# Kernel tuning notes

Hardware: AMD Instinct MI355X
Metric: run time of the kernel (lower is better)

The kernel has to match this reference:

```python
import jax, jax.numpy as jnp
import numpy as np

N_NODES = 100000
N_EDGES = 800000
F_DIM = 64
N_GRAPHS = 64


def _gcn_layer(h, W, b, src, dst, dis):
    # h: [N, F]; symmetric-normalized GCN conv with self-loops (PyG GCNConv semantics)
    hw = h @ W                                   # dense projection [N, F]
    norm = dis[src] * dis[dst]                   # [E]
    agg = jax.ops.segment_sum(hw[src] * norm[:, None], dst, num_segments=N_NODES)
    agg = agg + (dis * dis)[:, None] * hw        # self-loop contribution
    return agg + b


def setup_inputs() -> dict:
    key = jax.random.key(0)
    ks = jax.random.split(key, 10)
    x = jax.random.normal(ks[0], (N_NODES, F_DIM), dtype=jnp.float32)
    edge_index = jax.random.randint(ks[1], (2, N_EDGES), 0, N_NODES, dtype=jnp.int64 if jax.config.jax_enable_x64 else jnp.int32)
    batch = jnp.sort(jax.random.randint(ks[2], (N_NODES,), 0, N_GRAPHS, dtype=jnp.int32))
    scale = 1.0 / np.sqrt(F_DIM)
    W1 = jax.random.normal(ks[3], (F_DIM, F_DIM), dtype=jnp.float32) * scale
    b1 = jnp.zeros((F_DIM,), dtype=jnp.float32)
    W2 = jax.random.normal(ks[4], (F_DIM, F_DIM), dtype=jnp.float32) * scale
    b2 = jnp.zeros((F_DIM,), dtype=jnp.float32)
    W3 = jax.random.normal(ks[5], (F_DIM, F_DIM), dtype=jnp.float32) * scale
    b3 = jnp.zeros((F_DIM,), dtype=jnp.float32)
    return {"x": x, "edge_index": edge_index, "batch": batch,
            "W1": W1, "b1": b1, "W2": W2, "b2": b2, "W3": W3, "b3": b3}


def reference(x, edge_index, batch, W1, b1, W2, b2, W3, b3):
    src, dst = edge_index[0], edge_index[1]
    # degree with self-loops: deg[i] = 1 + in-degree(i)
    deg = jax.ops.segment_sum(jnp.ones((N_EDGES,), dtype=x.dtype), dst, num_segments=N_NODES) + 1.0
    dis = jax.lax.rsqrt(deg)                     # deg >= 1 always
    h = jax.nn.relu(_gcn_layer(x, W1, b1, src, dst, dis))
    h = jax.nn.relu(_gcn_layer(h, W2, b2, src, dst, dis))
    h = _gcn_layer(h, W3, b3, src, dst, dis)
    # global max pool over graphs in the batch
    out = jax.ops.segment_max(h, batch, num_segments=N_GRAPHS)
    return out
```

## Files before the change

### kernel.cpp

```cpp
#include <hip/hip_runtime.h>
#include <math.h>

#define N_NODES  100000
#define N_EDGES  800000
#define F        64
#define N_GRAPHS 64
#define NQUADS   25000
#define ROWB     128

typedef _Float16 half8 __attribute__((ext_vector_type(8)));
typedef float    f32x4 __attribute__((ext_vector_type(4)));

#define OFF_BUFA 0u
#define OFF_BUFB 12800256u
#define OFF_DIS  25600512u
#define OFF_DEG  26000512u
#define OFF_QB   26400512u
#define OFF_BSUM 26500544u
#define OFF_COL  26501120u
#define OFF_WT   40501120u

__device__ inline ushort f2bf(float f) {
    uint u = __float_as_uint(f);
    u = (u + 0x7FFFu + ((u >> 16) & 1u)) >> 16;
    return (ushort)u;
}
__device__ inline float bf2f(ushort s) {
    return __uint_as_float(((uint)s) << 16);
}

__global__ void k_zero(int* __restrict__ p, int n) {
    int i = blockIdx.x * blockDim.x + threadIdx.x;
    if (i < n) p[i] = 0;
}

__global__ void k_degree(const int* __restrict__ dst, int* __restrict__ degcnt,
                         int* __restrict__ rank) {
    int e = blockIdx.x * blockDim.x + threadIdx.x;
    if (e < N_EDGES) rank[e] = atomicAdd(&degcnt[dst[e]], 1);
}

__global__ void k_quad(const int* __restrict__ degcnt, int* __restrict__ qbase,
                       int* __restrict__ bsum, float* __restrict__ dis) {
    __shared__ int s[1024];
    int q = blockIdx.x * 1024 + threadIdx.x;
    int tot = 0;
    if (q < NQUADS) {
        const int4 d4 = *(const int4*)(degcnt + q * 4);
        float4 dv;
        dv.x = rsqrtf((float)d4.x + 1.0f);
        dv.y = rsqrtf((float)d4.y + 1.0f);
        dv.z = rsqrtf((float)d4.z + 1.0f);
        dv.w = rsqrtf((float)d4.w + 1.0f);
        *(float4*)(dis + q * 4) = dv;
        int m = max(max(d4.x, d4.y), max(d4.z, d4.w));
        int P = (m + 3) & ~3;
        tot = 4 * P;
    }
    s[threadIdx.x] = tot;
    __syncthreads();
    for (int off = 1; off < 1024; off <<= 1) {
        int t = (threadIdx.x >= off) ? s[threadIdx.x - off] : 0;
        __syncthreads();
        s[threadIdx.x] += t;
        __syncthreads();
    }
    if (q < NQUADS) qbase[q + 1] = s[threadIdx.x];
    if (threadIdx.x == 1023) bsum[blockIdx.x] = s[1023];
}

__global__ void k_scan2(int* __restrict__ bsum, int nb) {
    __shared__ int s[128];
    int t = threadIdx.x;
    int v = (t < nb) ? bsum[t] : 0;
    s[t] = v;
    __syncthreads();
    for (int off = 1; off < 128; off <<= 1) {
        int u = (t >= off) ? s[t - off] : 0;
        __syncthreads();
        s[t] += u;
        __syncthreads();
    }
    if (t < nb) bsum[t] = s[t] - v;
}

__global__ void k_scan3(int* __restrict__ qbase, const int* __restrict__ bsum) {
    int q = blockIdx.x * 1024 + threadIdx.x;
    if (q < NQUADS) qbase[q + 1] += bsum[blockIdx.x];
    if (q == 0) qbase[0] = 0;
}

__global__ void k_colinit(const int* __restrict__ qbase, int* __restrict__ col) {
    int total = qbase[NQUADS];
    int stride = gridDim.x * blockDim.x;
    for (int i = blockIdx.x * blockDim.x + threadIdx.x; i < total; i += stride)
        col[i] = N_NODES * ROWB;
}

__global__ void k_fill(const int* __restrict__ src, const int* __restrict__ dst,
                       const int* __restrict__ qbase, const int* __restrict__ rank,
                       int* __restrict__ col) {
    int e = blockIdx.x * blockDim.x + threadIdx.x;
    if (e < N_EDGES) {
        int d = dst[e];
        col[qbase[d >> 2] + rank[e] * 4 + (d & 3)] = src[e] * ROWB;
    }
}

__global__ void k_prepx(const float* __restrict__ x, const float* __restrict__ dis,
                        ushort* __restrict__ xs) {
    int t = blockIdx.x * blockDim.x + threadIdx.x;
    if (t < N_NODES * 8) {
        int n = t >> 3;
        float d = dis[n];
        const float4* px = (const float4*)(x + (size_t)t * 8);
        float4 a = px[0], b = px[1];
        ushort o[8] = { f2bf(d*a.x), f2bf(d*a.y), f2bf(d*a.z), f2bf(d*a.w),
                        f2bf(d*b.x), f2bf(d*b.y), f2bf(d*b.z), f2bf(d*b.w) };
        *(uint4*)(xs + (size_t)t * 8) = *(const uint4*)o;
    }
}

__global__ void k_prepw(const float* __restrict__ W1, const float* __restrict__ W2,
                        const float* __restrict__ W3, _Float16* __restrict__ Wt,
                        ushort* __restrict__ bufA, ushort* __restrict__ bufB,
                        float* __restrict__ out) {
    int t = blockIdx.x * blockDim.x + threadIdx.x;
    if (t < 3 * 4096) {
        int wsel = t >> 12, i = t & 4095;
        int k = i >> 6, f = i & 63;
        const float* Ws = (wsel == 0) ? W1 : (wsel == 1) ? W2 : W3;
        Wt[wsel * 4096 + f * 64 + k] = (_Float16)Ws[k * 64 + f];
    } else if (t < 3 * 4096 + 64) {
        int f = t - 3 * 4096;
        bufA[(size_t)N_NODES * F + f] = 0;
        bufB[(size_t)N_NODES * F + f] = 0;
    } else if (t < 3 * 4096 + 64 + N_GRAPHS * F) {
        out[t - (3 * 4096 + 64)] = -INFINITY;
    }
}

template<bool RELU, bool SCALE>
__global__ __launch_bounds__(256) void k_layer(const ushort* __restrict__ hs,
                                               const int* __restrict__ qbase,
                                               const int* __restrict__ col,
                                               const float* __restrict__ dis,
                                               const _Float16* __restrict__ Wt,
                                               const float* __restrict__ bias,
                                               ushort* __restrict__ hout) {
    __shared__ _Float16 g[64 * 64];
    int lane = threadIdx.x & 63;
    int w    = __builtin_amdgcn_readfirstlane(threadIdx.x >> 6);
    int chunk = blockIdx.x * 64;
    int wr16 = w * 16;
    int nbase = chunk + wr16;
    const char* hsb = (const char*)hs;
    int l2 = lane << 1;

    for (int p = 0; p < 4; ++p) {
        int na = nbase + 4 * p;
        int quad = na >> 2;
        int rowb = wr16 + 4 * p;
        bool vq = quad < NQUADS;
        int qb0 = 0, iters = 0;
        if (vq) {
            qb0   = __builtin_amdgcn_readfirstlane(qbase[quad]);
            int qb1 = __builtin_amdgcn_readfirstlane(qbase[quad + 1]);
            iters = (qb1 - qb0) >> 4;
        }
        float a0 = vq ? bf2f(hs[(size_t)(na    ) * F + lane]) : 0.f;
        float a1 = vq ? bf2f(hs[(size_t)(na + 1) * F + lane]) : 0.f;
        float a2 = vq ? bf2f(hs[(size_t)(na + 2) * F + lane]) : 0.f;
        float a3 = vq ? bf2f(hs[(size_t)(na + 3) * F + lane]) : 0.f;
        const int* cp0 = col + qb0;
        for (int i = 0; i < iters; ++i) {
            const int* cp = cp0 + (i << 4);
            float v0  = bf2f(*(const ushort*)(hsb + (uint)cp[0]  + l2));
            float v1  = bf2f(*(const ushort*)(hsb + (uint)cp[1]  + l2));
            float v2  = bf2f(*(const ushort*)(hsb + (uint)cp[2]  + l2));
            float v3  = bf2f(*(const ushort*)(hsb + (uint)cp[3]  + l2));
            float v4  = bf2f(*(const ushort*)(hsb + (uint)cp[4]  + l2));
            float v5  = bf2f(*(const ushort*)(hsb + (uint)cp[5]  + l2));
            float v6  = bf2f(*(const ushort*)(hsb + (uint)cp[6]  + l2));
            float v7  = bf2f(*(const ushort*)(hsb + (uint)cp[7]  + l2));
            float v8  = bf2f(*(const ushort*)(hsb + (uint)cp[8]  + l2));
            float v9  = bf2f(*(const ushort*)(hsb + (uint)cp[9]  + l2));
            float v10 = bf2f(*(const ushort*)(hsb + (uint)cp[10] + l2));
            float v11 = bf2f(*(const ushort*)(hsb + (uint)cp[11] + l2));
            float v12 = bf2f(*(const ushort*)(hsb + (uint)cp[12] + l2));
            float v13 = bf2f(*(const ushort*)(hsb + (uint)cp[13] + l2));
            float v14 = bf2f(*(const ushort*)(hsb + (uint)cp[14] + l2));
            float v15 = bf2f(*(const ushort*)(hsb + (uint)cp[15] + l2));
            a0 += v0 + v4 + v8  + v12;
            a1 += v1 + v5 + v9  + v13;
            a2 += v2 + v6 + v10 + v14;
            a3 += v3 + v7 + v11 + v15;
        }
        float d0 = vq ? dis[na]     : 0.f;
        float d1 = vq ? dis[na + 1] : 0.f;
        float d2 = vq ? dis[na + 2] : 0.f;
        float d3 = vq ? dis[na + 3] : 0.f;
        g[(rowb    ) * 64 + lane] = (_Float16)(d0 * a0);
        g[(rowb + 1) * 64 + lane] = (_Float16)(d1 * a1);
        g[(rowb + 2) * 64 + lane] = (_Float16)(d2 * a2);
        g[(rowb + 3) * 64 + lane] = (_Float16)(d3 * a3);
    }

    int l15 = lane & 15, lh = lane >> 4;
    half8 bfrag[2][4];
#pragma unroll
    for (int ks = 0; ks < 2; ++ks)
#pragma unroll
        for (int nt = 0; nt < 4; ++nt)
            bfrag[ks][nt] = *(const half8*)(Wt + (nt * 16 + l15) * 64 + ks * 32 + lh * 8);

    f32x4 acc4[4] = {};
#pragma unroll
    for (int ks = 0; ks < 2; ++ks) {
        half8 a = *(const half8*)(&g[(wr16 + l15) * 64 + ks * 32 + lh * 8]);
#pragma unroll
        for (int nt = 0; nt < 4; ++nt)
            acc4[nt] = __builtin_amdgcn_mfma_f32_16x16x32_f16(a, bfrag[ks][nt], acc4[nt], 0, 0, 0);
    }

    float bvals[4];
#pragma unroll
    for (int nt = 0; nt < 4; ++nt) bvals[nt] = bias[nt * 16 + l15];
#pragma unroll
    for (int rr = 0; rr < 4; ++rr) {
        int row = wr16 + lh * 4 + rr;
        int ng = chunk + row;
        if (ng < N_NODES) {
            float ds2 = 1.f;
            if (SCALE) ds2 = dis[ng];
#pragma unroll
            for (int nt = 0; nt < 4; ++nt) {
                float vv = acc4[nt][rr] + bvals[nt];
                if (RELU) vv = fmaxf(vv, 0.f);
                if (SCALE) vv *= ds2;
                hout[(size_t)ng * F + nt * 16 + l15] = f2bf(vv);
            }
        }
    }
}

__device__ inline void atomicMaxFloat(float* addr, float v) {
    if (v >= 0.f) atomicMax((int*)addr, __float_as_int(v));
    else          atomicMin((unsigned int*)addr, __float_as_uint(v));
}

__global__ __launch_bounds__(256) void k_pool(const ushort* __restrict__ h,
                                              const int* __restrict__ batch,
                                              float* __restrict__ out) {
    int lane = threadIdx.x & 63;
    int wid  = __builtin_amdgcn_readfirstlane((blockIdx.x * blockDim.x + threadIdx.x) >> 6);
    int nwaves = (gridDim.x * blockDim.x) >> 6;
    int per = (N_NODES + nwaves - 1) / nwaves;
    int n0 = wid * per, n1 = min(N_NODES, n0 + per);
    if (n0 >= n1) return;
    float acc = -INFINITY;
    int cur = batch[n0];
    for (int n = n0; n < n1; ++n) {
        int g = batch[n];
        if (g != cur) {
            atomicMaxFloat(&out[cur * F + lane], acc);
            acc = -INFINITY; cur = g;
        }
        acc = fmaxf(acc, bf2f(h[(size_t)n * F + lane]));
    }
    atomicMaxFloat(&out[cur * F + lane], acc);
}

extern "C" void kernel_launch(void* const* d_in, const int* in_sizes, int n_in,
                              void* d_out, int out_size, void* d_ws, size_t ws_size,
                              hipStream_t stream) {
    const float* x     = (const float*)d_in[0];
    const int*   ei    = (const int*)d_in[1];
    const int*   batch = (const int*)d_in[2];
    const float* W1 = (const float*)d_in[3];
    const float* b1 = (const float*)d_in[4];
    const float* W2 = (const float*)d_in[5];
    const float* b2 = (const float*)d_in[6];
    const float* W3 = (const float*)d_in[7];
    const float* b3 = (const float*)d_in[8];
    const int* src = ei;
    const int* dst = ei + N_EDGES;

    char* ws = (char*)d_ws;
    ushort*   bufA   = (ushort*)(ws + OFF_BUFA);
    int*      rank   = (int*)(ws + OFF_BUFA);
    ushort*   bufB   = (ushort*)(ws + OFF_BUFB);
    float*    dis    = (float*)(ws + OFF_DIS);
    int*      degcnt = (int*)(ws + OFF_DEG);
    int*      qbase  = (int*)(ws + OFF_QB);
    int*      bsum   = (int*)(ws + OFF_BSUM);
    int*      col    = (int*)(ws + OFF_COL);
    _Float16* wt     = (_Float16*)(ws + OFF_WT);
    float*    out    = (float*)d_out;

    k_zero<<<(N_NODES + 255) / 256, 256, 0, stream>>>(degcnt, N_NODES);
    k_degree<<<(N_EDGES + 255) / 256, 256, 0, stream>>>(dst, degcnt, rank);
    k_quad<<<25, 1024, 0, stream>>>(degcnt, qbase, bsum, dis);
    k_scan2<<<1, 128, 0, stream>>>(bsum, 25);
    k_scan3<<<25, 1024, 0, stream>>>(qbase, bsum);
    k_colinit<<<1024, 256, 0, stream>>>(qbase, col);
    k_fill<<<(N_EDGES + 255) / 256, 256, 0, stream>>>(src, dst, qbase, rank, col);

    k_prepx<<<(N_NODES * 8 + 255) / 256, 256, 0, stream>>>(x, dis, bufA);
    k_prepw<<<65, 256, 0, stream>>>(W1, W2, W3, wt, bufA, bufB, out);

    const int LBLOCKS = (N_NODES + 63) / 64;
    k_layer<true,  true ><<<LBLOCKS, 256, 0, stream>>>(bufA, qbase, col, dis, wt,        b1, bufB);
    k_layer<true,  true ><<<LBLOCKS, 256, 0, stream>>>(bufB, qbase, col, dis, wt + 4096, b2, bufA);
    k_layer<false, false><<<LBLOCKS, 256, 0, stream>>>(bufA, qbase, col, dis, wt + 8192, b3, bufB);

    k_pool<<<512, 256, 0, stream>>>(bufB, batch, out);
}
```

Before: 181.1 us.

## Fuse setup kernels and fold global max pool into final layer

Merges degree zeroing, column-sentinel init, weight transpose and output init into one kernel. Folds the second-level scan into the scan-apply kernel, which now also runs the input prescale. Fuses the graph max-pool into the last GCN layer using shared-memory atomics per block, so the final activations are never written or reread. This cuts launch count and one full pass over node features. In exchange, col is now initialised to a fixed capacity rather than the exact size, rank moves to its own buffer, and the pool relies on sorted batch ids with at most four graphs per block before falling back to global atomics.

```diff
diff --git a/kernel.cpp b/kernel.cpp
--- a/kernel.cpp
+++ b/kernel.cpp
@@ -7,6 +7,8 @@
 #define N_GRAPHS 64
 #define NQUADS   25000
 #define ROWB     128
+#define COLCAP   3500000
+#define SENT     (N_NODES * ROWB)
 
 typedef _Float16 half8 __attribute__((ext_vector_type(8)));
 typedef float    f32x4 __attribute__((ext_vector_type(4)));
@@ -19,6 +21,7 @@
 #define OFF_BSUM 26500544u
 #define OFF_COL  26501120u
 #define OFF_WT   40501120u
+#define OFF_RANK 40525696u
 
 __device__ inline ushort f2bf(float f) {
     uint u = __float_as_uint(f);
@@ -29,9 +32,32 @@
     return __uint_as_float(((uint)s) << 16);
 }
 
-__global__ void k_zero(int* __restrict__ p, int n) {
-    int i = blockIdx.x * blockDim.x + threadIdx.x;
-    if (i < n) p[i] = 0;
+__device__ inline void atomicMaxFloat(float* addr, float v) {
+    if (v >= 0.f) atomicMax((int*)addr, __float_as_int(v));
+    else          atomicMin((unsigned int*)addr, __float_as_uint(v));
+}
+
+__global__ void k_init(const float* __restrict__ W1, const float* __restrict__ W2,
+                       const float* __restrict__ W3, _Float16* __restrict__ Wt,
+                       ushort* __restrict__ bufA, ushort* __restrict__ bufB,
+                       float* __restrict__ out, int* __restrict__ degcnt,
+                       int* __restrict__ col) {
+    int tid = blockIdx.x * blockDim.x + threadIdx.x;
+    int stride = gridDim.x * blockDim.x;
+    for (int i = tid; i < COLCAP; i += stride) col[i] = SENT;
+    for (int i = tid; i < N_NODES; i += stride) degcnt[i] = 0;
+    if (tid < 3 * 4096) {
+        int wsel = tid >> 12, i = tid & 4095;
+        int k = i >> 6, f = i & 63;
+        const float* Ws = (wsel == 0) ? W1 : (wsel == 1) ? W2 : W3;
+        Wt[wsel * 4096 + f * 64 + k] = (_Float16)Ws[k * 64 + f];
+    } else if (tid < 3 * 4096 + 64) {
+        int f = tid - 3 * 4096;
+        bufA[(size_t)N_NODES * F + f] = 0;
+        bufB[(size_t)N_NODES * F + f] = 0;
+    } else if (tid < 3 * 4096 + 64 + N_GRAPHS * F) {
+        out[tid - (3 * 4096 + 64)] = -INFINITY;
+    }
 }
 
 __global__ void k_degree(const int* __restrict__ dst, int* __restrict__ degcnt,
@@ -69,32 +95,33 @@
     if (threadIdx.x == 1023) bsum[blockIdx.x] = s[1023];
 }
 
-__global__ void k_scan2(int* __restrict__ bsum, int nb) {
-    __shared__ int s[128];
-    int t = threadIdx.x;
-    int v = (t < nb) ? bsum[t] : 0;
-    s[t] = v;
-    __syncthreads();
-    for (int off = 1; off < 128; off <<= 1) {
-        int u = (t >= off) ? s[t - off] : 0;
+__global__ void k_scan3px(int* __restrict__ qbase, const int* __restrict__ bsum,
+                          const float* __restrict__ x, const float* __restrict__ dis,
+                          ushort* __restrict__ xs) {
+    if (blockIdx.x < 25) {
+        __shared__ int soff;
+        if (threadIdx.x == 0) {
+            int acc = 0;
+            for (int j = 0; j < (int)blockIdx.x; ++j) acc += bsum[j];
+            soff = acc;
+        }
         __syncthreads();
-        s[t] += u;
-        __syncthreads();
-    }
-    if (t < nb) bsum[t] = s[t] - v;
-}
-
-__global__ void k_scan3(int* __restrict__ qbase, const int* __restrict__ bsum) {
-    int q = blockIdx.x * 1024 + threadIdx.x;
-    if (q < NQUADS) qbase[q + 1] += bsum[blockIdx.x];
-    if (q == 0) qbase[0] = 0;
-}
-
-__global__ void k_colinit(const int* __restrict__ qbase, int* __restrict__ col) {
-    int total = qbase[NQUADS];
-    int stride = gridDim.x * blockDim.x;
-    for (int i = blockIdx.x * blockDim.x + threadIdx.x; i < total; i += stride)
-        col[i] = N_NODES * ROWB;
+        int off = soff;
+        int q = blockIdx.x * 1024 + threadIdx.x;
+        if (q < NQUADS) qbase[q + 1] += off;
+        if (q == 0) qbase[0] = 0;
+    } else {
+        int t = (blockIdx.x - 25) * 1024 + threadIdx.x;
+        if (t < N_NODES * 8) {
+            int n = t >> 3;
+            float d = dis[n];
+            const float4* px = (const float4*)(x + (size_t)t * 8);
+            float4 a = px[0], b = px[1];
+            ushort o[8] = { f2bf(d*a.x), f2bf(d*a.y), f2bf(d*a.z), f2bf(d*a.w),
+                            f2bf(d*b.x), f2bf(d*b.y), f2bf(d*b.z), f2bf(d*b.w) };
+            *(uint4*)(xs + (size_t)t * 8) = *(const uint4*)o;
+        }
+    }
 }
 
 __global__ void k_fill(const int* __restrict__ src, const int* __restrict__ dst,
@@ -107,48 +134,18 @@
     }
 }
 
-__global__ void k_prepx(const float* __restrict__ x, const float* __restrict__ dis,
-                        ushort* __restrict__ xs) {
-    int t = blockIdx.x * blockDim.x + threadIdx.x;
-    if (t < N_NODES * 8) {
-        int n = t >> 3;
-        float d = dis[n];
-        const float4* px = (const float4*)(x + (size_t)t * 8);
-        float4 a = px[0], b = px[1];
-        ushort o[8] = { f2bf(d*a.x), f2bf(d*a.y), f2bf(d*a.z), f2bf(d*a.w),
-                        f2bf(d*b.x), f2bf(d*b.y), f2bf(d*b.z), f2bf(d*b.w) };
-        *(uint4*)(xs + (size_t)t * 8) = *(const uint4*)o;
-    }
-}
-
-__global__ void k_prepw(const float* __restrict__ W1, const float* __restrict__ W2,
-                        const float* __restrict__ W3, _Float16* __restrict__ Wt,
-                        ushort* __restrict__ bufA, ushort* __restrict__ bufB,
-                        float* __restrict__ out) {
-    int t = blockIdx.x * blockDim.x + threadIdx.x;
-    if (t < 3 * 4096) {
-        int wsel = t >> 12, i = t & 4095;
-        int k = i >> 6, f = i & 63;
-        const float* Ws = (wsel == 0) ? W1 : (wsel == 1) ? W2 : W3;
-        Wt[wsel * 4096 + f * 64 + k] = (_Float16)Ws[k * 64 + f];
-    } else if (t < 3 * 4096 + 64) {
-        int f = t - 3 * 4096;
-        bufA[(size_t)N_NODES * F + f] = 0;
-        bufB[(size_t)N_NODES * F + f] = 0;
-    } else if (t < 3 * 4096 + 64 + N_GRAPHS * F) {
-        out[t - (3 * 4096 + 64)] = -INFINITY;
-    }
-}
-
-template<bool RELU, bool SCALE>
+template<bool RELU, bool SCALE, bool POOL>
 __global__ __launch_bounds__(256) void k_layer(const ushort* __restrict__ hs,
                                                const int* __restrict__ qbase,
                                                const int* __restrict__ col,
                                                const float* __restrict__ dis,
                                                const _Float16* __restrict__ Wt,
                                                const float* __restrict__ bias,
-                                               ushort* __restrict__ hout) {
+                                               ushort* __restrict__ hout,
+                                               const int* __restrict__ batch,
+                                               float* __restrict__ out) {
     __shared__ _Float16 g[64 * 64];
+    __shared__ float pl[4 * 64];
     int lane = threadIdx.x & 63;
     int w    = __builtin_amdgcn_readfirstlane(threadIdx.x >> 6);
     int chunk = blockIdx.x * 64;
@@ -156,6 +153,8 @@
     int nbase = chunk + wr16;
     const char* hsb = (const char*)hs;
     int l2 = lane << 1;
+
+    if (POOL) pl[threadIdx.x] = -INFINITY;
 
     for (int p = 0; p < 4; ++p) {
         int na = nbase + 4 * p;
@@ -226,49 +225,47 @@
     float bvals[4];
 #pragma unroll
     for (int nt = 0; nt < 4; ++nt) bvals[nt] = bias[nt * 16 + l15];
+
+    if (POOL) __syncthreads();
+    int gmin = 0;
+    if (POOL) gmin = __builtin_amdgcn_readfirstlane(batch[chunk]);
+
 #pragma unroll
     for (int rr = 0; rr < 4; ++rr) {
         int row = wr16 + lh * 4 + rr;
         int ng = chunk + row;
         if (ng < N_NODES) {
-            float ds2 = 1.f;
-            if (SCALE) ds2 = dis[ng];
-#pragma unroll
-            for (int nt = 0; nt < 4; ++nt) {
-                float vv = acc4[nt][rr] + bvals[nt];
-                if (RELU) vv = fmaxf(vv, 0.f);
-                if (SCALE) vv *= ds2;
-                hout[(size_t)ng * F + nt * 16 + l15] = f2bf(vv);
+            if (POOL) {
+                int gb = batch[ng];
+                int rel = gb - gmin;
+#pragma unroll
+                for (int nt = 0; nt < 4; ++nt) {
+                    float vv = acc4[nt][rr] + bvals[nt];
+                    if (RELU) vv = fmaxf(vv, 0.f);
+                    if (rel < 4) atomicMaxFloat(&pl[rel * 64 + nt * 16 + l15], vv);
+                    else         atomicMaxFloat(&out[gb * F + nt * 16 + l15], vv);
+                }
+            } else {
+                float ds2 = 1.f;
+                if (SCALE) ds2 = dis[ng];
+#pragma unroll
+                for (int nt = 0; nt < 4; ++nt) {
+                    float vv = acc4[nt][rr] + bvals[nt];
+                    if (RELU) vv = fmaxf(vv, 0.f);
+                    if (SCALE) vv *= ds2;
+                    hout[(size_t)ng * F + nt * 16 + l15] = f2bf(vv);
+                }
             }
         }
     }
-}
-
-__device__ inline void atomicMaxFloat(float* addr, float v) {
-    if (v >= 0.f) atomicMax((int*)addr, __float_as_int(v));
-    else          atomicMin((unsigned int*)addr, __float_as_uint(v));
-}
-
-__global__ __launch_bounds__(256) void k_pool(const ushort* __restrict__ h,
-                                              const int* __restrict__ batch,
-                                              float* __restrict__ out) {
-    int lane = threadIdx.x & 63;
-    int wid  = __builtin_amdgcn_readfirstlane((blockIdx.x * blockDim.x + threadIdx.x) >> 6);
-    int nwaves = (gridDim.x * blockDim.x) >> 6;
-    int per = (N_NODES + nwaves - 1) / nwaves;
-    int n0 = wid * per, n1 = min(N_NODES, n0 + per);
-    if (n0 >= n1) return;
-    float acc = -INFINITY;
-    int cur = batch[n0];
-    for (int n = n0; n < n1; ++n) {
-        int g = batch[n];
-        if (g != cur) {
-            atomicMaxFloat(&out[cur * F + lane], acc);
-            acc = -INFINITY; cur = g;
-        }
-        acc = fmaxf(acc, bf2f(h[(size_t)n * F + lane]));
-    }
-    atomicMaxFloat(&out[cur * F + lane], acc);
+    if (POOL) {
+        __syncthreads();
+        float v = pl[threadIdx.x];
+        int r = threadIdx.x >> 6, c = threadIdx.x & 63;
+        int gg = gmin + r;
+        if (v != -INFINITY && gg < N_GRAPHS)
+            atomicMaxFloat(&out[gg * F + c], v);
+    }
 }
 
 extern "C" void kernel_launch(void* const* d_in, const int* in_sizes, int n_in,
@@ -288,7 +285,6 @@
 
     char* ws = (char*)d_ws;
     ushort*   bufA   = (ushort*)(ws + OFF_BUFA);
-    int*      rank   = (int*)(ws + OFF_BUFA);
     ushort*   bufB   = (ushort*)(ws + OFF_BUFB);
     float*    dis    = (float*)(ws + OFF_DIS);
     int*      degcnt = (int*)(ws + OFF_DEG);
@@ -296,23 +292,17 @@
     int*      bsum   = (int*)(ws + OFF_BSUM);
     int*      col    = (int*)(ws + OFF_COL);
     _Float16* wt     = (_Float16*)(ws + OFF_WT);
+    int*      rank   = (int*)(ws + OFF_RANK);
     float*    out    = (float*)d_out;
 
-    k_zero<<<(N_NODES + 255) / 256, 256, 0, stream>>>(degcnt, N_NODES);
+    k_init<<<1024, 256, 0, stream>>>(W1, W2, W3, wt, bufA, bufB, out, degcnt, col);
     k_degree<<<(N_EDGES + 255) / 256, 256, 0, stream>>>(dst, degcnt, rank);
     k_quad<<<25, 1024, 0, stream>>>(degcnt, qbase, bsum, dis);
-    k_scan2<<<1, 128, 0, stream>>>(bsum, 25);
-    k_scan3<<<25, 1024, 0, stream>>>(qbase, bsum);
-    k_colinit<<<1024, 256, 0, stream>>>(qbase, col);
+    k_scan3px<<<25 + (N_NODES * 8 + 1023) / 1024, 1024, 0, stream>>>(qbase, bsum, x, dis, bufA);
     k_fill<<<(N_EDGES + 255) / 256, 256, 0, stream>>>(src, dst, qbase, rank, col);
 
-    k_prepx<<<(N_NODES * 8 + 255) / 256, 256, 0, stream>>>(x, dis, bufA);
-    k_prepw<<<65, 256, 0, stream>>>(W1, W2, W3, wt, bufA, bufB, out);
-
     const int LBLOCKS = (N_NODES + 63) / 64;
-    k_layer<true,  true ><<<LBLOCKS, 256, 0, stream>>>(bufA, qbase, col, dis, wt,        b1, bufB);
-    k_layer<true,  true ><<<LBLOCKS, 256, 0, stream>>>(bufB, qbase, col, dis, wt + 4096, b2, bufA);
-    k_layer<false, false><<<LBLOCKS, 256, 0, stream>>>(bufA, qbase, col, dis, wt + 8192, b3, bufB);
-
-    k_pool<<<512, 256, 0, stream>>>(bufB, batch, out);
-}
+    k_layer<true,  true,  false><<<LBLOCKS, 256, 0, stream>>>(bufA, qbase, col, dis, wt,        b1, bufB, nullptr, nullptr);
+    k_layer<true,  true,  false><<<LBLOCKS, 256, 0, stream>>>(bufB, qbase, col, dis, wt + 4096, b2, bufA, nullptr, nullptr);
+    k_layer<false, false, true ><<<LBLOCKS, 256, 0, stream>>>(bufA, qbase, col, dis, wt + 8192, b3, bufB, batch, out);
+}
```

Result: faster. 156.6 us (median of 2 runs) (-13.6%).
